# Performance work log

Hardware: AMD Instinct MI355X
Metric: run time of the kernel (lower is better)

## Reference

```python
import jax, jax.numpy as jnp
import numpy as np

VOCAB = 50000
EMBED = 128
CONTENT = 200
HIDDEN = 1024
LABELS = 2
BATCH = 4096


def setup_inputs() -> dict:
    key = jax.random.key(0)
    k_x, k_emb, k_w1, k_b1, k_w2, k_b2 = jax.random.split(key, 6)
    x = jax.random.randint(k_x, (BATCH, CONTENT), 0, VOCAB, dtype=jnp.int64)
    emb_table = jax.random.normal(k_emb, (VOCAB, EMBED), dtype=jnp.float32)
    fan_in1 = EMBED * CONTENT
    w1 = jax.random.uniform(k_w1, (HIDDEN, fan_in1), dtype=jnp.float32,
                            minval=-1.0, maxval=1.0) / np.sqrt(fan_in1)
    b1 = jax.random.uniform(k_b1, (HIDDEN,), dtype=jnp.float32,
                            minval=-1.0, maxval=1.0) / np.sqrt(fan_in1)
    w2 = jax.random.uniform(k_w2, (LABELS, HIDDEN), dtype=jnp.float32,
                            minval=-1.0, maxval=1.0) / np.sqrt(HIDDEN)
    b2 = jax.random.uniform(k_b2, (LABELS,), dtype=jnp.float32,
                            minval=-1.0, maxval=1.0) / np.sqrt(HIDDEN)
    return {"x": x, "emb_table": emb_table, "w1": w1, "b1": b1,
            "w2": w2, "b2": b2}


def reference(x, emb_table, w1, b1, w2, b2):
    # padding_idx=0: row 0 of the embedding table is zero
    table = emb_table.at[0].set(0.0)
    emb = table[x]                                   # [B, C, E]
    flat = emb.reshape(emb.shape[0], -1)             # [B, C*E]
    h = jax.nn.relu(flat @ w1.T + b1)                # [B, H]
    logits = h @ w2.T + b2                           # [B, L]
    # Softmax(dim=0) on a 1-D per-sample vector == softmax over labels
    return jax.nn.softmax(logits, axis=-1)
```

## Files before the change

kernel.cpp:

```cpp
#include <hip/hip_runtime.h>
#include <hip/hip_bf16.h>
#include <stdint.h>

#define BATCH   4096
#define CONTENT 200
#define EMBED   128
#define HIDDEN  1024
#define KDIM    (CONTENT*EMBED)
#define KSTEPS64 (KDIM/64)
#define SPLITK  2
#define KCHUNK64 200

typedef __bf16 bf16_t;
typedef __bf16 bf16x8 __attribute__((ext_vector_type(8)));
typedef float  f32x4  __attribute__((ext_vector_type(4)));

#define WS_EMBT  0ull
#define WS_W1    12800000ull
#define WS_HP    65228800ull
#define HP_STRIDE 4194304ull

__device__ __forceinline__ void gload_lds16(const void* g, void* l) {
  __builtin_amdgcn_global_load_lds(
      (const __attribute__((address_space(1))) uint32_t*)g,
      (__attribute__((address_space(3))) uint32_t*)l, 16, 0, 0);
}

__global__ __launch_bounds__(256) void k_prep(const float* __restrict__ emb,
                                              const float* __restrict__ w1,
                                              bf16_t* __restrict__ embT,
                                              bf16_t* __restrict__ w1T) {
  if (blockIdx.x < 320) {
    const int NU = 800000;
    int stride = 320 * 256;
    for (int u = blockIdx.x * 256 + threadIdx.x; u < NU; u += stride) {
      const float4* s = (const float4*)(emb + (size_t)u * 8);
      float4 f0 = s[0], f1 = s[1];
      float sc = (u >> 4) == 0 ? 0.0f : 1.0f;
      bf16x8 r;
      r[0]=(bf16_t)(f0.x*sc); r[1]=(bf16_t)(f0.y*sc); r[2]=(bf16_t)(f0.z*sc); r[3]=(bf16_t)(f0.w*sc);
      r[4]=(bf16_t)(f1.x*sc); r[5]=(bf16_t)(f1.y*sc); r[6]=(bf16_t)(f1.z*sc); r[7]=(bf16_t)(f1.w*sc);
      *(bf16x8*)(embT + (size_t)u * 8) = r;
    }
  } else {
    const long long NU = 3276800;
    long long stride = 2048LL * 256;
    for (long long u = (long long)(blockIdx.x - 320) * 256 + threadIdx.x; u < NU; u += stride) {
      const float4* s = (const float4*)(w1 + u * 8);
      float4 f0 = s[0], f1 = s[1];
      bf16x8 r;
      r[0]=(bf16_t)f0.x; r[1]=(bf16_t)f0.y; r[2]=(bf16_t)f0.z; r[3]=(bf16_t)f0.w;
      r[4]=(bf16_t)f1.x; r[5]=(bf16_t)f1.y; r[6]=(bf16_t)f1.z; r[7]=(bf16_t)f1.w;
      *(bf16x8*)(w1T + u * 8) = r;
    }
  }
}

__global__ __launch_bounds__(256) void k_gemm(const int* __restrict__ x,
                                              const bf16_t* __restrict__ embT,
                                              const bf16_t* __restrict__ W,
                                              float* __restrict__ hp) {
  __shared__ char smem[65536];
  const int tid = threadIdx.x;
  const int w = tid >> 6, l = tid & 63;
  const int m0 = blockIdx.x * 128;
  const int n0 = blockIdx.y * 128;
  const int chunk = blockIdx.z;
  const int ks_begin = chunk * KCHUNK64;
  const int nt = KCHUNK64;

  const int rbase = tid >> 3;
  const int sg = (tid & 7) ^ (rbase & 7);
  const char* embB = (const char*)embT;
  const char* Wb = (const char*)W;

  const char* bsrc[4];
  #pragma unroll
  for (int rd = 0; rd < 4; ++rd)
    bsrc[rd] = Wb + (size_t)(n0 + rd * 32 + rbase) * (KDIM * 2)
                  + (size_t)ks_begin * 128 + sg * 16;

  int tokc = ks_begin >> 1;
  int xv[4], xn[4];
  #pragma unroll
  for (int rd = 0; rd < 4; ++rd)
    xv[rd] = x[(m0 + rd * 32 + rbase) * CONTENT + tokc];
  #pragma unroll
  for (int rd = 0; rd < 4; ++rd)
    xn[rd] = x[(m0 + rd * 32 + rbase) * CONTENT + tokc + 1];

#define ISSUE(koff, base)                                                     \
  { _Pragma("unroll")                                                         \
    for (int rd = 0; rd < 4; ++rd) {                                          \
      gload_lds16(embB + (size_t)xv[rd] * 256 + (koff) + sg * 16,             \
                  smem + (base) + w * 1024 + rd * 4096);                      \
      gload_lds16(bsrc[rd], smem + (base) + 16384 + w * 1024 + rd * 4096);    \
      bsrc[rd] += 128;                                                        \
    } }

  const int wr = w >> 1, wc = w & 1;
  const int lane_r = l & 15;
  const int g = l >> 4;

  f32x4 acc[4][4];
  #pragma unroll
  for (int i = 0; i < 4; ++i)
    #pragma unroll
    for (int j = 0; j < 4; ++j)
      acc[i][j] = (f32x4){0.f, 0.f, 0.f, 0.f};

  ISSUE(0, 0);
  ISSUE(128, 32768);
  __syncthreads();

  for (int t = 0; t < nt; ++t) {
    const char* AsB = smem + ((t & 1) << 15);
    const char* BsB = AsB + 16384;

    #pragma unroll
    for (int kk = 0; kk < 2; ++kk) {
      bf16x8 af[4], bfr[4];
      #pragma unroll
      for (int i = 0; i < 4; ++i) {
        int rowa = wr * 64 + i * 16 + lane_r;
        int rowb = wc * 64 + i * 16 + lane_r;
        int slot = ((kk << 2) | g) ^ (lane_r & 7);
        af[i]  = *(const bf16x8*)(AsB + rowa * 128 + slot * 16);
        bfr[i] = *(const bf16x8*)(BsB + rowb * 128 + slot * 16);
      }
      __builtin_amdgcn_s_setprio(1);
      #pragma unroll
      for (int i = 0; i < 4; ++i)
        #pragma unroll
        for (int j = 0; j < 4; ++j)
          acc[i][j] = __builtin_amdgcn_mfma_f32_16x16x32_bf16(af[i], bfr[j], acc[i][j], 0, 0, 0);
      __builtin_amdgcn_s_setprio(0);
    }

    __syncthreads();

    int tt = t + 2;
    if (tt < nt) {
      int ks = ks_begin + tt;
      if ((ks & 1) == 0) {
        tokc = ks >> 1;
        #pragma unroll
        for (int rd = 0; rd < 4; ++rd) xv[rd] = xn[rd];
        int nxt = tokc + 1; if (nxt > CONTENT - 1) nxt = CONTENT - 1;
        #pragma unroll
        for (int rd = 0; rd < 4; ++rd)
          xn[rd] = x[(m0 + rd * 32 + rbase) * CONTENT + nxt];
      }
      ISSUE((ks & 1) << 7, (t & 1) << 15);
    }
  }
#undef ISSUE

  float* hout = hp + (size_t)chunk * HP_STRIDE;
  const int colBase = n0 + wc * 64 + lane_r;
  const int rowBase = m0 + wr * 64 + (l >> 4) * 4;
  #pragma unroll
  for (int i = 0; i < 4; ++i)
    #pragma unroll
    for (int j = 0; j < 4; ++j)
      #pragma unroll
      for (int r = 0; r < 4; ++r)
        hout[(size_t)(rowBase + i * 16 + r) * HIDDEN + colBase + j * 16] = acc[i][j][r];
}

__global__ __launch_bounds__(256) void k_final(const float* __restrict__ hp,
                                               const float* __restrict__ b1,
                                               const float* __restrict__ w2,
                                               const float* __restrict__ b2,
                                               float* __restrict__ out) {
  const int tid = threadIdx.x;
  const int w = tid >> 6, l = tid & 63;
  const int m = blockIdx.x * 4 + w;
  const float* r0 = hp + (size_t)m * HIDDEN;
  const float* r1 = r0 + HP_STRIDE;
  float l0 = 0.f, l1 = 0.f;
  #pragma unroll
  for (int t = 0; t < 4; ++t) {
    int j = t * 256 + l * 4;
    float4 p0 = *(const float4*)(r0 + j);
    float4 p1 = *(const float4*)(r1 + j);
    float4 bb = *(const float4*)(b1 + j);
    float4 wa = *(const float4*)(w2 + j);
    float4 wb = *(const float4*)(w2 + HIDDEN + j);
    float h;
    h = p0.x + p1.x + bb.x; h = fmaxf(h, 0.f); l0 += h * wa.x; l1 += h * wb.x;
    h = p0.y + p1.y + bb.y; h = fmaxf(h, 0.f); l0 += h * wa.y; l1 += h * wb.y;
    h = p0.z + p1.z + bb.z; h = fmaxf(h, 0.f); l0 += h * wa.z; l1 += h * wb.z;
    h = p0.w + p1.w + bb.w; h = fmaxf(h, 0.f); l0 += h * wa.w; l1 += h * wb.w;
  }
  #pragma unroll
  for (int off = 32; off > 0; off >>= 1) {
    l0 += __shfl_xor(l0, off, 64);
    l1 += __shfl_xor(l1, off, 64);
  }
  if (l == 0) {
    float z0 = l0 + b2[0], z1 = l1 + b2[1];
    float mx = fmaxf(z0, z1);
    float e0 = expf(z0 - mx), e1 = expf(z1 - mx);
    float s = 1.f / (e0 + e1);
    out[2 * m]     = e0 * s;
    out[2 * m + 1] = e1 * s;
  }
}

extern "C" void kernel_launch(void* const* d_in, const int* in_sizes, int n_in,
                              void* d_out, int out_size, void* d_ws, size_t ws_size,
                              hipStream_t stream) {
  (void)in_sizes; (void)n_in; (void)out_size; (void)ws_size;
  const int*   x   = (const int*)d_in[0];
  const float* emb = (const float*)d_in[1];
  const float* w1  = (const float*)d_in[2];
  const float* b1  = (const float*)d_in[3];
  const float* w2  = (const float*)d_in[4];
  const float* b2  = (const float*)d_in[5];
  float* out = (float*)d_out;
  char* ws = (char*)d_ws;
  bf16_t* embT = (bf16_t*)(ws + WS_EMBT);
  bf16_t* Wbf  = (bf16_t*)(ws + WS_W1);
  float*  hp   = (float*)(ws + WS_HP);

  hipLaunchKernelGGL(k_prep,  dim3(2368), dim3(256), 0, stream, emb, w1, embT, Wbf);
  hipLaunchKernelGGL(k_gemm,  dim3(BATCH/128, HIDDEN/128, SPLITK), dim3(256), 0, stream,
                     x, embT, Wbf, hp);
  hipLaunchKernelGGL(k_final, dim3(BATCH/4), dim3(256), 0, stream, hp, b1, w2, b2, out);
}
```

Baseline: 435.0 us.

## Use 256x256 tiles with 8 waves, split-K 4 and phased async pipeline

Rewrites the gather-GEMM kernel to use 256x256 output tiles per 512-thread block with split-K of 4 (256 blocks). It remaps block IDs for XCD-aware placement and double-buffers 64KB LDS stages. Loads are interleaved into eight compute phases separated by barriers and explicit vmcnt waits. The final kernel now sums four partials. The aim is more data reuse per tile and better overlap of gathers with MFMA, at the cost of larger LDS use, more registers and extra partial-sum traffic.

```diff
diff --git a/kernel.cpp b/kernel.cpp
--- a/kernel.cpp
+++ b/kernel.cpp
@@ -7,9 +7,7 @@
 #define EMBED   128
 #define HIDDEN  1024
 #define KDIM    (CONTENT*EMBED)
-#define KSTEPS64 (KDIM/64)
-#define SPLITK  2
-#define KCHUNK64 200
+#define SPLITK  4
 
 typedef __bf16 bf16_t;
 typedef __bf16 bf16x8 __attribute__((ext_vector_type(8)));
@@ -56,116 +54,139 @@
   }
 }
 
-__global__ __launch_bounds__(256) void k_gemm(const int* __restrict__ x,
-                                              const bf16_t* __restrict__ embT,
-                                              const bf16_t* __restrict__ W,
-                                              float* __restrict__ hp) {
-  __shared__ char smem[65536];
+__global__ __launch_bounds__(512, 2) void k_gemm(const int* __restrict__ x,
+                                                 const bf16_t* __restrict__ embT,
+                                                 const bf16_t* __restrict__ W,
+                                                 float* __restrict__ hp) {
+  __shared__ char smem[131072];
   const int tid = threadIdx.x;
-  const int w = tid >> 6, l = tid & 63;
-  const int m0 = blockIdx.x * 128;
-  const int n0 = blockIdx.y * 128;
-  const int chunk = blockIdx.z;
-  const int ks_begin = chunk * KCHUNK64;
-  const int nt = KCHUNK64;
-
-  const int rbase = tid >> 3;
-  const int sg = (tid & 7) ^ (rbase & 7);
+  const int wid = tid >> 6, l = tid & 63;
+  const int orig = (blockIdx.x & 7) * 32 + (blockIdx.x >> 3);
+  const int m0 = (orig & 15) * 256;
+  const int n0 = ((orig >> 4) & 3) * 256;
+  const int chunk = orig >> 6;
+  const int cb100 = chunk * 100;
+  const int T0 = chunk * 50;
+
+  const int sg16 = ((l & 7) ^ (l >> 3)) * 16;
   const char* embB = (const char*)embT;
   const char* Wb = (const char*)W;
-
-  const char* bsrc[4];
-  #pragma unroll
-  for (int rd = 0; rd < 4; ++rd)
-    bsrc[rd] = Wb + (size_t)(n0 + rd * 32 + rbase) * (KDIM * 2)
-                  + (size_t)ks_begin * 128 + sg * 16;
-
-  int tokc = ks_begin >> 1;
-  int xv[4], xn[4];
-  #pragma unroll
-  for (int rd = 0; rd < 4; ++rd)
-    xv[rd] = x[(m0 + rd * 32 + rbase) * CONTENT + tokc];
-  #pragma unroll
-  for (int rd = 0; rd < 4; ++rd)
-    xn[rd] = x[(m0 + rd * 32 + rbase) * CONTENT + tokc + 1];
-
-#define ISSUE(koff, base)                                                     \
-  { _Pragma("unroll")                                                         \
-    for (int rd = 0; rd < 4; ++rd) {                                          \
-      gload_lds16(embB + (size_t)xv[rd] * 256 + (koff) + sg * 16,             \
-                  smem + (base) + w * 1024 + rd * 4096);                      \
-      gload_lds16(bsrc[rd], smem + (base) + 16384 + w * 1024 + rd * 4096);    \
-      bsrc[rd] += 128;                                                        \
-    } }
-
-  const int wr = w >> 1, wc = w & 1;
-  const int lane_r = l & 15;
-  const int g = l >> 4;
-
-  f32x4 acc[4][4];
-  #pragma unroll
-  for (int i = 0; i < 4; ++i)
+  const int wq = wid >> 2, wm = wid & 3;
+  size_t brow[2];
+  #pragma unroll
+  for (int rd = 0; rd < 2; ++rd)
+    brow[rd] = (size_t)(n0 + rd*128 + wq*64 + wm*8 + (l>>3)) * (size_t)(KDIM*2) + sg16;
+  int xrow[4];
+  #pragma unroll
+  for (int f = 0; f < 4; ++f)
+    xrow[f] = (m0 + (f>>1)*128 + (f&1)*64 + (tid>>3)) * CONTENT;
+
+  const int wr = wq, wc = wm;
+  const int lane_r = l & 15, g = l >> 4;
+  const int aoff = wr*16384 + lane_r*128;
+  const int boff = 32768 + wc*8192 + lane_r*128;
+  const int s0 = ((0*4 + g) ^ (lane_r & 7)) * 16;
+  const int s1 = ((1*4 + g) ^ (lane_r & 7)) * 16;
+
+#define ISSUE_A(BUF, H, XA, KOFF)                                             \
+  { gload_lds16(embB + (size_t)XA[0*2+(H)]*256 + (KOFF) + sg16,               \
+                smem + (BUF) + 0*16384 + (H)*8192 + wid*1024);                \
+    gload_lds16(embB + (size_t)XA[1*2+(H)]*256 + (KOFF) + sg16,               \
+                smem + (BUF) + 1*16384 + (H)*8192 + wid*1024); }
+#define ISSUE_B(BUF, H, LT)                                                   \
+  { const int lt_ = (LT) > 99 ? 99 : (LT);                                    \
+    const size_t ko_ = (size_t)(cb100 + lt_) * 128 + (H)*1638400u;            \
+    gload_lds16(Wb + brow[0] + ko_,                                           \
+                smem + (BUF) + 32768 + 0*16384 + wq*8192 + (H)*4096 + wm*1024); \
+    gload_lds16(Wb + brow[1] + ko_,                                           \
+                smem + (BUF) + 32768 + 1*16384 + wq*8192 + (H)*4096 + wm*1024); }
+
+#define PHASE(IH, JH, CB, ISSUE_STMT, TAIL)                                   \
+  { bf16x8 af[4][2], bfr[2][2];                                               \
+    _Pragma("unroll")                                                         \
+    for (int ii = 0; ii < 4; ++ii) {                                          \
+      af[ii][0] = *(const bf16x8*)(smem + (CB) + aoff + (IH)*8192 + ii*2048 + s0); \
+      af[ii][1] = *(const bf16x8*)(smem + (CB) + aoff + (IH)*8192 + ii*2048 + s1); \
+    }                                                                         \
+    _Pragma("unroll")                                                         \
+    for (int jj = 0; jj < 2; ++jj) {                                          \
+      bfr[jj][0] = *(const bf16x8*)(smem + (CB) + boff + (JH)*4096 + jj*2048 + s0); \
+      bfr[jj][1] = *(const bf16x8*)(smem + (CB) + boff + (JH)*4096 + jj*2048 + s1); \
+    }                                                                         \
+    ISSUE_STMT                                                                \
+    __builtin_amdgcn_s_barrier();                                             \
+    asm volatile("s_waitcnt lgkmcnt(0)" ::: "memory");                        \
+    __builtin_amdgcn_s_setprio(1);                                            \
+    _Pragma("unroll")                                                         \
+    for (int ii = 0; ii < 4; ++ii)                                            \
+      _Pragma("unroll")                                                       \
+      for (int jj = 0; jj < 2; ++jj) {                                        \
+        acc[(IH)*4+ii][(JH)*2+jj] = __builtin_amdgcn_mfma_f32_16x16x32_bf16(  \
+            af[ii][0], bfr[jj][0], acc[(IH)*4+ii][(JH)*2+jj], 0, 0, 0);       \
+        acc[(IH)*4+ii][(JH)*2+jj] = __builtin_amdgcn_mfma_f32_16x16x32_bf16(  \
+            af[ii][1], bfr[jj][1], acc[(IH)*4+ii][(JH)*2+jj], 0, 0, 0);       \
+      }                                                                       \
+    __builtin_amdgcn_s_setprio(0);                                            \
+    TAIL                                                                      \
+    __builtin_amdgcn_s_barrier(); }
+
+  f32x4 acc[8][4];
+  #pragma unroll
+  for (int i = 0; i < 8; ++i)
     #pragma unroll
     for (int j = 0; j < 4; ++j)
       acc[i][j] = (f32x4){0.f, 0.f, 0.f, 0.f};
 
-  ISSUE(0, 0);
-  ISSUE(128, 32768);
-  __syncthreads();
-
-  for (int t = 0; t < nt; ++t) {
-    const char* AsB = smem + ((t & 1) << 15);
-    const char* BsB = AsB + 16384;
-
-    #pragma unroll
-    for (int kk = 0; kk < 2; ++kk) {
-      bf16x8 af[4], bfr[4];
-      #pragma unroll
-      for (int i = 0; i < 4; ++i) {
-        int rowa = wr * 64 + i * 16 + lane_r;
-        int rowb = wc * 64 + i * 16 + lane_r;
-        int slot = ((kk << 2) | g) ^ (lane_r & 7);
-        af[i]  = *(const bf16x8*)(AsB + rowa * 128 + slot * 16);
-        bfr[i] = *(const bf16x8*)(BsB + rowb * 128 + slot * 16);
-      }
-      __builtin_amdgcn_s_setprio(1);
-      #pragma unroll
-      for (int i = 0; i < 4; ++i)
-        #pragma unroll
-        for (int j = 0; j < 4; ++j)
-          acc[i][j] = __builtin_amdgcn_mfma_f32_16x16x32_bf16(af[i], bfr[j], acc[i][j], 0, 0, 0);
-      __builtin_amdgcn_s_setprio(0);
-    }
-
-    __syncthreads();
-
-    int tt = t + 2;
-    if (tt < nt) {
-      int ks = ks_begin + tt;
-      if ((ks & 1) == 0) {
-        tokc = ks >> 1;
-        #pragma unroll
-        for (int rd = 0; rd < 4; ++rd) xv[rd] = xn[rd];
-        int nxt = tokc + 1; if (nxt > CONTENT - 1) nxt = CONTENT - 1;
-        #pragma unroll
-        for (int rd = 0; rd < 4; ++rd)
-          xn[rd] = x[(m0 + rd * 32 + rbase) * CONTENT + nxt];
-      }
-      ISSUE((ks & 1) << 7, (t & 1) << 15);
-    }
-  }
-#undef ISSUE
+  int xcur[4], xnxt[4];
+  #pragma unroll
+  for (int f = 0; f < 4; ++f) xcur[f] = x[xrow[f] + T0];
+  #pragma unroll
+  for (int f = 0; f < 4; ++f) xnxt[f] = x[xrow[f] + T0 + 1];
+  ISSUE_A(0, 0, xcur, 0)
+  ISSUE_A(0, 1, xcur, 0)
+  ISSUE_B(0, 0, 0)
+  ISSUE_B(0, 1, 0)
+  ISSUE_A(65536, 0, xcur, 128)
+  ISSUE_B(65536, 0, 1)
+  asm volatile("s_waitcnt vmcnt(4)" ::: "memory");
+  __builtin_amdgcn_s_barrier();
+
+  for (int j = 0; j < 50; ++j) {
+    int tnew = T0 + j + 2; if (tnew > CONTENT - 1) tnew = CONTENT - 1;
+    int xnew[4];
+    #pragma unroll
+    for (int f = 0; f < 4; ++f) xnew[f] = x[xrow[f] + tnew];
+
+    PHASE(0,0, 0,     { ISSUE_A(65536, 1, xcur, 128); }, {})
+    PHASE(0,1, 0,     { ISSUE_B(65536, 1, 2*j+1); }, {})
+    PHASE(1,0, 0,     { ISSUE_A(0, 0, xnxt, 0); }, {})
+    PHASE(1,1, 0,     { ISSUE_B(0, 0, 2*j+2); },
+                      { asm volatile("s_waitcnt vmcnt(4)" ::: "memory"); })
+    PHASE(0,0, 65536, { ISSUE_A(0, 1, xnxt, 0); }, {})
+    PHASE(0,1, 65536, { ISSUE_B(0, 1, 2*j+2); }, {})
+    PHASE(1,0, 65536, { ISSUE_A(65536, 0, xnxt, 128); }, {})
+    PHASE(1,1, 65536, { ISSUE_B(65536, 0, 2*j+3); },
+                      { asm volatile("s_waitcnt vmcnt(4)" ::: "memory"); })
+
+    #pragma unroll
+    for (int f = 0; f < 4; ++f) { xcur[f] = xnxt[f]; xnxt[f] = xnew[f]; }
+  }
+#undef PHASE
+#undef ISSUE_A
+#undef ISSUE_B
+
+  asm volatile("s_waitcnt vmcnt(0)" ::: "memory");
 
   float* hout = hp + (size_t)chunk * HP_STRIDE;
   const int colBase = n0 + wc * 64 + lane_r;
-  const int rowBase = m0 + wr * 64 + (l >> 4) * 4;
-  #pragma unroll
-  for (int i = 0; i < 4; ++i)
-    #pragma unroll
-    for (int j = 0; j < 4; ++j)
+  const int rowBase = m0 + wr * 128 + (l >> 4) * 4;
+  #pragma unroll
+  for (int i = 0; i < 8; ++i)
+    #pragma unroll
+    for (int jj = 0; jj < 4; ++jj)
       #pragma unroll
       for (int r = 0; r < 4; ++r)
-        hout[(size_t)(rowBase + i * 16 + r) * HIDDEN + colBase + j * 16] = acc[i][j][r];
+        hout[(size_t)(rowBase + i * 16 + r) * HIDDEN + colBase + jj * 16] = acc[i][jj][r];
 }
 
 __global__ __launch_bounds__(256) void k_final(const float* __restrict__ hp,
@@ -178,20 +199,24 @@
   const int m = blockIdx.x * 4 + w;
   const float* r0 = hp + (size_t)m * HIDDEN;
   const float* r1 = r0 + HP_STRIDE;
+  const float* r2 = r1 + HP_STRIDE;
+  const float* r3 = r2 + HP_STRIDE;
   float l0 = 0.f, l1 = 0.f;
   #pragma unroll
   for (int t = 0; t < 4; ++t) {
     int j = t * 256 + l * 4;
     float4 p0 = *(const float4*)(r0 + j);
     float4 p1 = *(const float4*)(r1 + j);
+    float4 p2 = *(const float4*)(r2 + j);
+    float4 p3 = *(const float4*)(r3 + j);
     float4 bb = *(const float4*)(b1 + j);
     float4 wa = *(const float4*)(w2 + j);
     float4 wb = *(const float4*)(w2 + HIDDEN + j);
     float h;
-    h = p0.x + p1.x + bb.x; h = fmaxf(h, 0.f); l0 += h * wa.x; l1 += h * wb.x;
-    h = p0.y + p1.y + bb.y; h = fmaxf(h, 0.f); l0 += h * wa.y; l1 += h * wb.y;
-    h = p0.z + p1.z + bb.z; h = fmaxf(h, 0.f); l0 += h * wa.z; l1 += h * wb.z;
-    h = p0.w + p1.w + bb.w; h = fmaxf(h, 0.f); l0 += h * wa.w; l1 += h * wb.w;
+    h = p0.x + p1.x + p2.x + p3.x + bb.x; h = fmaxf(h, 0.f); l0 += h * wa.x; l1 += h * wb.x;
+    h = p0.y + p1.y + p2.y + p3.y + bb.y; h = fmaxf(h, 0.f); l0 += h * wa.y; l1 += h * wb.y;
+    h = p0.z + p1.z + p2.z + p3.z + bb.z; h = fmaxf(h, 0.f); l0 += h * wa.z; l1 += h * wb.z;
+    h = p0.w + p1.w + p2.w + p3.w + bb.w; h = fmaxf(h, 0.f); l0 += h * wa.w; l1 += h * wb.w;
   }
   #pragma unroll
   for (int off = 32; off > 0; off >>= 1) {
@@ -225,7 +250,6 @@
   float*  hp   = (float*)(ws + WS_HP);
 
   hipLaunchKernelGGL(k_prep,  dim3(2368), dim3(256), 0, stream, emb, w1, embT, Wbf);
-  hipLaunchKernelGGL(k_gemm,  dim3(BATCH/128, HIDDEN/128, SPLITK), dim3(256), 0, stream,
-                     x, embT, Wbf, hp);
+  hipLaunchKernelGGL(k_gemm,  dim3(256), dim3(512), 0, stream, x, embT, Wbf, hp);
   hipLaunchKernelGGL(k_final, dim3(BATCH/4), dim3(256), 0, stream, hp, b1, w2, b2, out);
 }
```

Result: faster. 391.6 us (-10.0%).
